# Kernel tuning notes

Measured on AMD Instinct MI355X. Metric: run time of the kernel, lower is better.

The kernel has to match this reference:

```python
import jax, jax.numpy as jnp
import numpy as np

# Straight-through binarization: forward sign(x) in {-1,+1}, backward hardtanh-style
# gradient clip (grad passes where |x| <= 1). Matches BinaryNet Binarize + BinaryTanh.
@jax.custom_vjp
def binarize(x):
    return jnp.where(x >= 0, 1.0, -1.0).astype(x.dtype)

def _bin_fwd(x):
    return binarize(x), x

def _bin_bwd(res, g):
    return (g * (jnp.abs(res) <= 1.0).astype(g.dtype),)

binarize.defvjp(_bin_fwd, _bin_bwd)

def conv_valid(x, w):
    # x: [B,C,H,W], w: [O,I,3,3], stride 1, no padding
    return jax.lax.conv_general_dilated(
        x, w, window_strides=(1, 1), padding='VALID',
        dimension_numbers=('NCHW', 'OIHW', 'NCHW'))


def setup_inputs() -> dict:
    key = jax.random.key(0)
    ks = jax.random.split(key, 6)
    B = 8192
    x = jax.random.normal(ks[0], (B, 1, 28, 28), dtype=jnp.float32)
    w1 = jax.random.normal(ks[1], (16, 1, 3, 3), dtype=jnp.float32) * 0.1
    w2 = jax.random.normal(ks[2], (32, 16, 3, 3), dtype=jnp.float32) * 0.1
    w3 = jax.random.normal(ks[3], (32, 32, 3, 3), dtype=jnp.float32) * 0.1
    wfc = jax.random.normal(ks[4], (10, 32 * 11 * 11), dtype=jnp.float32) * 0.1
    bfc = jax.random.normal(ks[5], (10,), dtype=jnp.float32) * 0.1
    return {'x': x, 'w1': w1, 'w2': w2, 'w3': w3, 'wfc': wfc, 'bfc': bfc}


def reference(x, w1, w2, w3, wfc, bfc):
    # BinaryConv2d: conv with sign(W); BinaryTanh: hardtanh then sign -> sign(x)
    h = binarize(conv_valid(x, binarize(w1)))   # [B,16,26,26]
    h = binarize(conv_valid(h, binarize(w2)))   # [B,32,24,24]
    h = binarize(conv_valid(h, binarize(w3)))   # [B,32,22,22]
    B, C, H, W = h.shape
    # AvgPool2d(2): reshape + mean (H,W divisible by 2)
    h = h.reshape(B, C, H // 2, 2, W // 2, 2).mean(axis=(3, 5))  # [B,32,11,11]
    h = h.reshape(B, -1)                                          # [B,3872]
    logits = h @ binarize(wfc).T + bfc                            # [B,10]
    return jax.nn.log_softmax(logits, axis=1)
```

## Files before the change

### kernel.cpp

```cpp
#include <hip/hip_runtime.h>
#include <cstdint>

typedef unsigned uint;
typedef unsigned short u16;
typedef int v4i  __attribute__((ext_vector_type(4)));
typedef int v16i __attribute__((ext_vector_type(16)));
typedef float v2f __attribute__((ext_vector_type(2)));

static constexpr int WS_W2B = 144;
static constexpr int WS_W3B = 1424;
static constexpr int WS_FC  = 3728;

static constexpr int L_XS  = 0;
static constexpr int L_H1  = 3136;
static constexpr int L_H2  = 0;
static constexpr int L_H2B = 18432;
static constexpr int L_H3  = 18432;
static constexpr int L_RED = 20736;
static constexpr int L_LG  = 20816;
static constexpr int L_TOT = 20856;

__device__ __host__ __forceinline__ int bitpos32(int c) {
    return (((c >> 2) & 1) << 4) + (c & 3) + ((c >> 3) << 2);
}

__global__ __launch_bounds__(256) void pack_kernel(
    const float* __restrict__ w1, const float* __restrict__ w2,
    const float* __restrict__ w3, const float* __restrict__ wfc,
    uint* __restrict__ wsu)
{
    int gid = blockIdx.x * 256 + threadIdx.x;
    if (gid < 144) {
        ((float*)wsu)[gid] = (w1[gid] >= 0.f) ? 1.f : -1.f;
    } else if (gid < 464) {
        int f = gid - 144, s = f >> 6, l = f & 63;
        int oc = l & 31, tap = s * 2 + (l >> 5);
        uint w[4] = {0u, 0u, 0u, 0u};
        if (tap < 9) {
            for (int e = 0; e < 16; ++e) {
                uint b = (w2[(oc * 16 + e) * 9 + tap] >= 0.f) ? 0x01u : 0xFFu;
                w[e >> 2] |= b << (8 * (e & 3));
            }
        }
        for (int j = 0; j < 4; ++j) wsu[WS_W2B + f * 4 + j] = w[j];
    } else if (gid < 1040) {
        int f = gid - 464, s = f >> 6, l = f & 63;
        int oc = l & 31, icb = (l >> 5) * 16;
        uint w[4] = {0u, 0u, 0u, 0u};
        for (int e = 0; e < 16; ++e) {
            uint b = (w3[(oc * 32 + icb + e) * 9 + s] >= 0.f) ? 0x01u : 0xFFu;
            w[e >> 2] |= b << (8 * (e & 3));
        }
        for (int j = 0; j < 4; ++j) wsu[WS_W3B + f * 4 + j] = w[j];
    } else if (gid < 5880) {
        int f = gid - 1040, o = f / 484, p = f % 484;
        int Y = p / 22, X = p % 22;
        const float* base = wfc + o * 3872 + (Y >> 1) * 11 + (X >> 1);
        uint bits = 0;
        for (int c = 0; c < 32; ++c)
            bits |= (base[c * 121] >= 0.f ? 1u : 0u) << bitpos32(c);
        wsu[WS_FC + f] = bits;
    }
}

__device__ __forceinline__ int expand4(uint t) {
    return (int)~(((t * 0x00204081u) & 0x01010101u) * 0xFEu);
}
__device__ __forceinline__ v4i expand16(uint bits) {
    v4i r;
    r[0] = expand4(bits & 0xFu);
    r[1] = expand4((bits >> 4) & 0xFu);
    r[2] = expand4((bits >> 8) & 0xFu);
    r[3] = expand4((bits >> 12) & 0xFu);
    return r;
}

__global__ __launch_bounds__(256) void binet_kernel(
    const float* __restrict__ x, const uint* __restrict__ wsu,
    const float* __restrict__ bfc, float* __restrict__ out)
{
    __shared__ __align__(16) unsigned char lds[L_TOT];
    const int t = threadIdx.x;
    const int img = blockIdx.x;
    const int l = t & 63, wave = t >> 6, half = l >> 5, lane31 = l & 31;

    float* xs = (float*)(lds + L_XS);
    signed char* h1 = (signed char*)(lds + L_H1);
    signed char* h2 = (signed char*)(lds + L_H2);
    u16*  h2u = (u16*)(lds + L_H2B);
    uint* h2w = (uint*)(lds + L_H2B);
    u16*  h3u = (u16*)(lds + L_H3);
    uint* h3  = (uint*)(lds + L_H3);
    uint (*red)[5] = (uint(*)[5])(lds + L_RED);
    float* lg = (float*)(lds + L_LG);

    {
        const float* xin = x + (size_t)img * 784;
        for (int i = t; i < 784; i += 256) xs[i] = xin[i];
    }
    __syncthreads();

    if (t < 234) {
        const float* wf = (const float*)wsu;
        const int g = t / 26, xcol = t - g * 26;
        const int y0 = 3 * g;
        float xv[5][3];
        #pragma unroll
        for (int r = 0; r < 5; ++r) {
            int rr = y0 + r; if (rr > 27) rr = 27;
            #pragma unroll
            for (int c = 0; c < 3; ++c)
                xv[r][c] = xs[rr*28 + xcol + c];
        }
        v2f xp[9];
        #pragma unroll
        for (int ky = 0; ky < 3; ++ky)
            #pragma unroll
            for (int kx = 0; kx < 3; ++kx) {
                v2f p; p.x = xv[ky][kx]; p.y = xv[ky+1][kx];
                xp[ky*3+kx] = p;
            }
        uint m0 = 0, m1 = 0, m2 = 0;
        for (int oc = 0; oc < 16; ++oc) {
            v2f s01 = {0.f, 0.f};
            float s2 = 0.f;
            #pragma unroll
            for (int ky = 0; ky < 3; ++ky)
                #pragma unroll
                for (int kx = 0; kx < 3; ++kx) {
                    float w = wf[oc*9 + ky*3 + kx];
                    s01 = xp[ky*3+kx] * w + s01;
                    s2  = fmaf(xv[ky + 2][kx], w, s2);
                }
            float s0 = s01.x, s1 = s01.y;
            bool b0 = (s0 >= 0.f), b1 = (s1 >= 0.f), b2 = (s2 >= 0.f);
            if (__builtin_expect((int)((fabsf(s0) < 1e-4f) |
                                       (fabsf(s1) < 1e-4f) |
                                       (fabsf(s2) < 1e-4f)), 0)) {
                double d0 = 0.0, d1 = 0.0, d2 = 0.0;
                for (int k = 0; k < 9; ++k) {
                    double w = (double)wf[oc*9 + k];
                    d0 += (double)xv[k/3    ][k%3] * w;
                    d1 += (double)xv[k/3 + 1][k%3] * w;
                    d2 += (double)xv[k/3 + 2][k%3] * w;
                }
                b0 = (d0 >= 0.0); b1 = (d1 >= 0.0); b2 = (d2 >= 0.0);
            }
            m0 |= (uint)b0 << oc;
            m1 |= (uint)b1 << oc;
            m2 |= (uint)b2 << oc;
        }
        *(v4i*)(h1 + ((y0    )*26 + xcol)*16) = expand16(m0);
        *(v4i*)(h1 + ((y0 + 1)*26 + xcol)*16) = expand16(m1);
        if (y0 + 2 <= 25)
            *(v4i*)(h1 + ((y0 + 2)*26 + xcol)*16) = expand16(m2);
    }
    __syncthreads();

    {
        const v4i* w2bp = (const v4i*)(wsu + WS_W2B);
        v4i b2f[5];
        #pragma unroll
        for (int s = 0; s < 5; ++s) b2f[s] = w2bp[s*64 + l];
        for (int tile = wave; tile < 18; tile += 4) {
            const int mb = tile * 32;
            const int row = mb + lane31;
            const int y = row / 24, xx = row % 24;
            v16i acc = {0,0,0,0,0,0,0,0,0,0,0,0,0,0,0,0};
            #pragma unroll
            for (int s = 0; s < 5; ++s) {
                int tap = s*2 + half; if (tap > 8) tap = 8;
                int ky = tap / 3, kx = tap - ky*3;
                v4i b = *(const v4i*)(h1 + ((y+ky)*26 + xx+kx)*16);
                acc = __builtin_amdgcn_mfma_i32_32x32x32_i8(b2f[s], b, acc, 0, 0, 0);
            }
            uint mneg = 0;
            #pragma unroll
            for (int r = 0; r < 16; ++r)
                mneg |= (((uint)acc[r]) >> 31) << r;
            h2u[row*2 + half] = (u16)~mneg;
        }
    }
    __syncthreads();

    for (int p = t; p < 576; p += 256) {
        uint w = h2w[p];
        v4i lo, hi;
        lo[0] = expand4( w        & 0xFu);
        lo[1] = expand4((w >> 16) & 0xFu);
        lo[2] = expand4((w >>  4) & 0xFu);
        lo[3] = expand4((w >> 20) & 0xFu);
        hi[0] = expand4((w >>  8) & 0xFu);
        hi[1] = expand4((w >> 24) & 0xFu);
        hi[2] = expand4((w >> 12) & 0xFu);
        hi[3] = expand4((w >> 28) & 0xFu);
        *(v4i*)(h2 + p*16)        = lo;
        *(v4i*)(h2 + 9216 + p*16) = hi;
    }
    __syncthreads();

    {
        const v4i* w3bp = (const v4i*)(wsu + WS_W3B);
        v4i b3f[9];
        #pragma unroll
        for (int s = 0; s < 9; ++s) b3f[s] = w3bp[s*64 + l];
        const signed char* h2h = h2 + half*9216;
        for (int tile = wave; tile < 16; tile += 4) {
            const int mb = tile * 32;
            int row = mb + lane31;
            int pr = (row < 484) ? row : 483;
            const int y = pr / 22, xx = pr % 22;
            v16i acc = {0,0,0,0,0,0,0,0,0,0,0,0,0,0,0,0};
            #pragma unroll
            for (int s = 0; s < 9; ++s) {
                const int ky = s / 3, kx = s - ky*3;
                v4i b = *(const v4i*)(h2h + ((y+ky)*24 + xx+kx)*16);
                acc = __builtin_amdgcn_mfma_i32_32x32x32_i8(b3f[s], b, acc, 0, 0, 0);
            }
            uint mneg = 0;
            #pragma unroll
            for (int r = 0; r < 16; ++r)
                mneg |= (((uint)acc[r]) >> 31) << r;
            if (row < 484) h3u[row*2 + half] = (u16)~mneg;
        }
    }
    __syncthreads();

    uint acc5[5] = {0u, 0u, 0u, 0u, 0u};
    for (int p = t; p < 484; p += 256) {
        uint h = h3[p];
        const uint* wp = wsu + WS_FC + p;
        #pragma unroll
        for (int o = 0; o < 5; ++o)
            acc5[o] += (uint)__popc(h ^ wp[(2*o)*484])
                     + ((uint)__popc(h ^ wp[(2*o+1)*484]) << 16);
    }
    #pragma unroll
    for (int o = 0; o < 5; ++o) {
        uint v = acc5[o];
        v += __shfl_down(v, 32); v += __shfl_down(v, 16);
        v += __shfl_down(v, 8);  v += __shfl_down(v, 4);
        v += __shfl_down(v, 2);  v += __shfl_down(v, 1);
        acc5[o] = v;
    }
    if (l == 0) {
        #pragma unroll
        for (int o = 0; o < 5; ++o) red[wave][o] = acc5[o];
    }
    __syncthreads();
    if (t < 10) {
        uint S = 0;
        #pragma unroll
        for (int j = 0; j < 4; ++j) {
            uint w = red[j][t >> 1];
            S += (t & 1) ? (w >> 16) : (w & 0xFFFFu);
        }
        lg[t] = 0.25f * (float)(15488 - 2*(int)S) + bfc[t];
    }
    __syncthreads();
    if (t < 10) {
        float m = lg[0];
        #pragma unroll
        for (int o = 1; o < 10; ++o) m = fmaxf(m, lg[o]);
        float se = 0.f;
        #pragma unroll
        for (int o = 0; o < 10; ++o) se += expf(lg[o] - m);
        out[(size_t)img*10 + t] = lg[t] - m - logf(se);
    }
}

extern "C" void kernel_launch(void* const* d_in, const int* in_sizes, int n_in,
                              void* d_out, int out_size, void* d_ws, size_t ws_size,
                              hipStream_t stream)
{
    const float* x   = (const float*)d_in[0];
    const float* w1  = (const float*)d_in[1];
    const float* w2  = (const float*)d_in[2];
    const float* w3  = (const float*)d_in[3];
    const float* wfc = (const float*)d_in[4];
    const float* bfc = (const float*)d_in[5];
    float* out = (float*)d_out;
    uint* wsu  = (uint*)d_ws;

    const int B = in_sizes[0] / 784;

    hipLaunchKernelGGL(pack_kernel, dim3(23), dim3(256), 0, stream,
                       w1, w2, w3, wfc, wsu);
    hipLaunchKernelGGL(binet_kernel, dim3(B), dim3(256), 0, stream,
                       x, wsu, bfc, out);
}
```

Baseline: 109.8 us.

## Use 2x2 output tiles in conv1 and shrink LDS footprint by aliasing buffers

Conv1 now has 169 threads each compute a 2x2 output block with packed float2 FMAs, replacing 234 threads computing 3 rows each. Each thread loads fewer inputs per output, and no work is wasted on the clamped last row. The packed h2 bitmask buffer is moved to overlap the h1 region, and the reduction/logit scratch is aliased to offset 0. To make the overlap safe, the expansion pass reads the packed words into registers and adds a barrier before writing. This lowers LDS per block, which may allow more blocks per CU, at the cost of an extra barrier.

Result: slower. 123.5 us (+12.5%).

```diff
diff --git a/kernel.cpp b/kernel.cpp
--- a/kernel.cpp
+++ b/kernel.cpp
@@ -14,11 +14,11 @@
 static constexpr int L_XS  = 0;
 static constexpr int L_H1  = 3136;
 static constexpr int L_H2  = 0;
-static constexpr int L_H2B = 18432;
+static constexpr int L_H2B = 13952;
 static constexpr int L_H3  = 18432;
-static constexpr int L_RED = 20736;
-static constexpr int L_LG  = 20816;
-static constexpr int L_TOT = 20856;
+static constexpr int L_RED = 0;
+static constexpr int L_LG  = 80;
+static constexpr int L_TOT = 20368;
 
 __device__ __host__ __forceinline__ int bitpos32(int c) {
     return (((c >> 2) & 1) << 4) + (c & 3) + ((c >> 3) << 2);
@@ -100,60 +100,64 @@
     }
     __syncthreads();
 
-    if (t < 234) {
+    if (t < 169) {
         const float* wf = (const float*)wsu;
-        const int g = t / 26, xcol = t - g * 26;
-        const int y0 = 3 * g;
-        float xv[5][3];
-        #pragma unroll
-        for (int r = 0; r < 5; ++r) {
-            int rr = y0 + r; if (rr > 27) rr = 27;
-            #pragma unroll
-            for (int c = 0; c < 3; ++c)
-                xv[r][c] = xs[rr*28 + xcol + c];
-        }
-        v2f xp[9];
+        const int g = t / 13, cc = (t - g * 13) * 2;
+        const int y0 = 2 * g;
+        v2f p[3][4];
         #pragma unroll
         for (int ky = 0; ky < 3; ++ky)
             #pragma unroll
-            for (int kx = 0; kx < 3; ++kx) {
-                v2f p; p.x = xv[ky][kx]; p.y = xv[ky+1][kx];
-                xp[ky*3+kx] = p;
-            }
-        uint m0 = 0, m1 = 0, m2 = 0;
+            for (int c = 0; c < 4; ++c) {
+                v2f q;
+                q.x = xs[(y0 + ky    )*28 + cc + c];
+                q.y = xs[(y0 + ky + 1)*28 + cc + c];
+                p[ky][c] = q;
+            }
+        uint m00 = 0, m10 = 0, m01 = 0, m11 = 0;
         for (int oc = 0; oc < 16; ++oc) {
-            v2f s01 = {0.f, 0.f};
-            float s2 = 0.f;
+            v2f sA = {0.f, 0.f}, sB = {0.f, 0.f};
             #pragma unroll
             for (int ky = 0; ky < 3; ++ky)
                 #pragma unroll
                 for (int kx = 0; kx < 3; ++kx) {
                     float w = wf[oc*9 + ky*3 + kx];
-                    s01 = xp[ky*3+kx] * w + s01;
-                    s2  = fmaf(xv[ky + 2][kx], w, s2);
+                    sA = p[ky][kx    ] * w + sA;
+                    sB = p[ky][kx + 1] * w + sB;
                 }
-            float s0 = s01.x, s1 = s01.y;
-            bool b0 = (s0 >= 0.f), b1 = (s1 >= 0.f), b2 = (s2 >= 0.f);
-            if (__builtin_expect((int)((fabsf(s0) < 1e-4f) |
-                                       (fabsf(s1) < 1e-4f) |
-                                       (fabsf(s2) < 1e-4f)), 0)) {
-                double d0 = 0.0, d1 = 0.0, d2 = 0.0;
+            bool b00 = (sA.x >= 0.f), b10 = (sA.y >= 0.f);
+            bool b01 = (sB.x >= 0.f), b11 = (sB.y >= 0.f);
+            float mx = fmaxf(fmaxf(fabsf(sA.x), fabsf(sA.y)),
+                             fmaxf(fabsf(sB.x), fabsf(sB.y)));
+            if (__builtin_expect(mx < 1e-4f, 0)) {
+                double rw[4][4];
+                for (int c = 0; c < 4; ++c) {
+                    rw[0][c] = (double)p[0][c].x;
+                    rw[1][c] = (double)p[1][c].x;
+                    rw[2][c] = (double)p[2][c].x;
+                    rw[3][c] = (double)p[2][c].y;
+                }
+                double d00 = 0.0, d10 = 0.0, d01 = 0.0, d11 = 0.0;
                 for (int k = 0; k < 9; ++k) {
+                    int ky = k / 3, kx = k - ky*3;
                     double w = (double)wf[oc*9 + k];
-                    d0 += (double)xv[k/3    ][k%3] * w;
-                    d1 += (double)xv[k/3 + 1][k%3] * w;
-                    d2 += (double)xv[k/3 + 2][k%3] * w;
+                    d00 += w * rw[ky    ][kx    ];
+                    d10 += w * rw[ky + 1][kx    ];
+                    d01 += w * rw[ky    ][kx + 1];
+                    d11 += w * rw[ky + 1][kx + 1];
                 }
-                b0 = (d0 >= 0.0); b1 = (d1 >= 0.0); b2 = (d2 >= 0.0);
-            }
-            m0 |= (uint)b0 << oc;
-            m1 |= (uint)b1 << oc;
-            m2 |= (uint)b2 << oc;
-        }
-        *(v4i*)(h1 + ((y0    )*26 + xcol)*16) = expand16(m0);
-        *(v4i*)(h1 + ((y0 + 1)*26 + xcol)*16) = expand16(m1);
-        if (y0 + 2 <= 25)
-            *(v4i*)(h1 + ((y0 + 2)*26 + xcol)*16) = expand16(m2);
+                b00 = (d00 >= 0.0); b10 = (d10 >= 0.0);
+                b01 = (d01 >= 0.0); b11 = (d11 >= 0.0);
+            }
+            m00 |= (uint)b00 << oc;
+            m10 |= (uint)b10 << oc;
+            m01 |= (uint)b01 << oc;
+            m11 |= (uint)b11 << oc;
+        }
+        *(v4i*)(h1 + ((y0    )*26 + cc    )*16) = expand16(m00);
+        *(v4i*)(h1 + ((y0    )*26 + cc + 1)*16) = expand16(m01);
+        *(v4i*)(h1 + ((y0 + 1)*26 + cc    )*16) = expand16(m10);
+        *(v4i*)(h1 + ((y0 + 1)*26 + cc + 1)*16) = expand16(m11);
     }
     __syncthreads();
 
@@ -183,19 +187,26 @@
     }
     __syncthreads();
 
-    for (int p = t; p < 576; p += 256) {
-        uint w = h2w[p];
-        v4i lo, hi;
-        lo[0] = expand4( w        & 0xFu);
-        lo[1] = expand4((w >> 16) & 0xFu);
-        lo[2] = expand4((w >>  4) & 0xFu);
-        lo[3] = expand4((w >> 20) & 0xFu);
-        hi[0] = expand4((w >>  8) & 0xFu);
-        hi[1] = expand4((w >> 24) & 0xFu);
-        hi[2] = expand4((w >> 12) & 0xFu);
-        hi[3] = expand4((w >> 28) & 0xFu);
-        *(v4i*)(h2 + p*16)        = lo;
-        *(v4i*)(h2 + 9216 + p*16) = hi;
+    {
+        uint wbuf[3];
+        int np = 0;
+        for (int p = t; p < 576; p += 256) wbuf[np++] = h2w[p];
+        __syncthreads();
+        np = 0;
+        for (int p = t; p < 576; p += 256) {
+            uint w = wbuf[np++];
+            v4i lo, hi;
+            lo[0] = expand4( w        & 0xFu);
+            lo[1] = expand4((w >> 16) & 0xFu);
+            lo[2] = expand4((w >>  4) & 0xFu);
+            lo[3] = expand4((w >> 20) & 0xFu);
+            hi[0] = expand4((w >>  8) & 0xFu);
+            hi[1] = expand4((w >> 24) & 0xFu);
+            hi[2] = expand4((w >> 12) & 0xFu);
+            hi[3] = expand4((w >> 28) & 0xFu);
+            *(v4i*)(h2 + p*16)        = lo;
+            *(v4i*)(h2 + 9216 + p*16) = hi;
+        }
     }
     __syncthreads();
 
```
